# Kernel optimization log

Measured on AMD Instinct MI355X. Metric: run time of the kernel, lower is better.

The kernel has to match this reference:

```python
import jax, jax.numpy as jnp
import numpy as np

NUM_GROUPS = 2
NUM_VARS = 320
CODE_DIM = 256  # per-group dim = 128
TAU = 2.0


def setup_inputs() -> dict:
    key = jax.random.key(0)
    k1, k2, k3, k4 = jax.random.split(key, 4)
    B, S, H = 4, 512, 512
    x = jax.random.normal(k1, (B, S, H), jnp.float32)
    W = jax.random.normal(k2, (H, NUM_GROUPS * NUM_VARS), jnp.float32) * 0.02
    b = jnp.zeros((NUM_GROUPS * NUM_VARS,), jnp.float32)
    codevectors = jax.random.normal(k3, (1, NUM_GROUPS * NUM_VARS, CODE_DIM // NUM_GROUPS), jnp.float32)
    # Gumbel(0,1) noise, matching -log(Exponential(1).sample) in the original
    u = jax.random.uniform(k4, (B * S * NUM_GROUPS, NUM_VARS), jnp.float32, 1e-6, 1.0 - 1e-6)
    gumbels = -jnp.log(-jnp.log(u))
    return {"x": x, "W": W, "b": b, "codevectors": codevectors, "gumbels": gumbels}


def reference(x, W, b, codevectors, gumbels):
    B, S, H = x.shape
    BS = B * S
    logits = x @ W + b                                    # [B, S, G*V]
    l = logits.reshape(BS * NUM_GROUPS, NUM_VARS)         # [BS*G, V]
    # gumbel-softmax, hard=True (straight-through)
    y_soft = jax.nn.softmax((l + gumbels) / TAU, axis=-1)
    idx = jnp.argmax(y_soft, axis=-1)
    y_hard = jax.nn.one_hot(idx, NUM_VARS, dtype=l.dtype)
    codevector_probs = y_hard - jax.lax.stop_gradient(y_soft) + y_soft
    # perplexity over the soft distribution of the raw logits (no gumbel, no tau)
    soft_dist = jax.nn.softmax(l.reshape(BS, NUM_GROUPS, NUM_VARS), axis=-1)
    marg = jnp.mean(soft_dist, axis=0)                    # [G, V]
    perp = jnp.sum(jnp.exp(-jnp.sum(marg * jnp.log(marg + 1e-7), axis=-1)))
    # dense broadcast-multiply-reduce codebook selection (as in the original)
    cp = codevector_probs.reshape(BS, NUM_GROUPS * NUM_VARS)        # [BS, G*V]
    cv = cp[:, :, None] * codevectors                                # [BS, G*V, D/G]
    cv = cv.reshape(BS, NUM_GROUPS, NUM_VARS, -1).sum(axis=-2)      # [BS, G, D/G]
    return cv.reshape(B, S, -1), perp
```

## Files before the change

kernel.cpp:

```cpp
#include <hip/hip_runtime.h>

#define NV 320
#define GV 640
#define DHALF 128
#define BSROWS 2048
#define K_DIM 512
#define LDA 40
#define NRED 40
#define NMT 128

typedef _Float16 half8 __attribute__((ext_vector_type(8)));
typedef float floatx4 __attribute__((ext_vector_type(4)));

#define MFMA16(a, b, c) __builtin_amdgcn_mfma_f32_16x16x32_f16(a, b, c, 0, 0, 0)

__global__ __launch_bounds__(256) void gemm_row_kernel(
    const float* __restrict__ X, const float* __restrict__ W,
    const float* __restrict__ bias, const float* __restrict__ gum,
    const float* __restrict__ cvs, float* __restrict__ out,
    float* __restrict__ part, int* __restrict__ counter) {
  __shared__ _Float16 Ah[2][16 * LDA], Al[2][16 * LDA];
  __shared__ float sm_m[4][16], sm_av[4][16], sm_s[4][16];
  __shared__ int sm_ai[4][16], sm_idx[16];

  const int tid = threadIdx.x;
  const int bid = blockIdx.x;
  if (bid == 0 && tid == 0) *counter = 0;
  const int g = bid & 1;
  const int mtile = bid >> 1;
  const int bm = mtile * 16;
  const int w = tid >> 6, lane = tid & 63;
  const int wcol0 = w * 80;
  const int gn0 = g * NV;

  const int srow = tid >> 4, skc = (tid & 15) << 1;
  const float* Xg = X + (bm + srow) * K_DIM + skc;
  const int sA = srow * LDA + skc;

  const int frow = lane & 15;
  const int rq0 = (lane >> 4) << 2;
  const int fkg = (lane >> 4) << 3;
  const float* Wf = W + gn0 + wcol0 + frow;

  float gv[5][4];
#pragma unroll
  for (int q = 0; q < 4; ++q) {
    const int r = bm + rq0 + q;
    const float* gr = gum + (2 * r + g) * NV + wcol0 + frow;
#pragma unroll
    for (int j = 0; j < 5; ++j) gv[j][q] = gr[j * 16];
  }

  floatx4 acc[5] = {};

  auto stageA = [&](int buf, float2 xv) {
#pragma unroll
    for (int j = 0; j < 2; ++j) {
      float s = ((j == 0) ? xv.x : xv.y) * 64.0f;
      _Float16 h = (_Float16)s;
      Ah[buf][sA + j] = h;
      Al[buf][sA + j] = (_Float16)(s - (float)h);
    }
  };
  auto loadW = [&](int k0, float (&wv)[5][8]) {
#pragma unroll
    for (int j = 0; j < 5; ++j)
#pragma unroll
      for (int kk = 0; kk < 8; ++kk)
        wv[j][kk] = Wf[(k0 + fkg + kk) * GV + j * 16];
  };
  auto computeTile = [&](int buf, const float (&wv)[5][8]) {
    half8 ah = *(const half8*)&Ah[buf][frow * LDA + fkg];
    half8 al = *(const half8*)&Al[buf][frow * LDA + fkg];
#pragma unroll
    for (int j = 0; j < 5; ++j) {
      half8 bh, bl;
#pragma unroll
      for (int kk = 0; kk < 8; ++kk) {
        float s = wv[j][kk] * 1024.0f;
        _Float16 h = (_Float16)s;
        bh[kk] = h;
        bl[kk] = (_Float16)(s - (float)h);
      }
      acc[j] = MFMA16(ah, bh, acc[j]);
      acc[j] = MFMA16(ah, bl, acc[j]);
      acc[j] = MFMA16(al, bh, acc[j]);
    }
  };

  float wvA[5][8], wvB[5][8];
  stageA(0, *(const float2*)(Xg));
  loadW(0, wvA);
  __syncthreads();

  for (int k0 = 0; k0 < K_DIM; k0 += 64) {
    const bool more = (k0 + 64) < K_DIM;

    float2 xv1 = *(const float2*)(Xg + k0 + 32);
    loadW(k0 + 32, wvB);
    computeTile(0, wvA);
    stageA(1, xv1);
    __syncthreads();

    float2 xv2;
    if (more) {
      xv2 = *(const float2*)(Xg + k0 + 64);
      loadW(k0 + 64, wvA);
    }
    computeTile(1, wvB);
    if (more) stageA(0, xv2);
    __syncthreads();
  }

  const float inv = 1.0f / 65536.0f;
#pragma unroll
  for (int j = 0; j < 5; ++j) {
    const float bb = bias[gn0 + wcol0 + j * 16 + frow];
#pragma unroll
    for (int q = 0; q < 4; ++q) acc[j][q] = acc[j][q] * inv + bb;
  }

  float m[4], bv[4];
  int bi[4];
#pragma unroll
  for (int q = 0; q < 4; ++q) {
    float mm = acc[0][q];
    float av = acc[0][q] + gv[0][q];
    int ai = wcol0 + frow;
#pragma unroll
    for (int j = 1; j < 5; ++j) {
      mm = fmaxf(mm, acc[j][q]);
      float a2 = acc[j][q] + gv[j][q];
      if (a2 > av) { av = a2; ai = wcol0 + j * 16 + frow; }
    }
#pragma unroll
    for (int o = 1; o < 16; o <<= 1) {
      mm = fmaxf(mm, __shfl_xor(mm, o));
      float ov = __shfl_xor(av, o);
      int oi = __shfl_xor(ai, o);
      if (ov > av || (ov == av && oi < ai)) { av = ov; ai = oi; }
    }
    m[q] = mm; bv[q] = av; bi[q] = ai;
  }
  if (frow == 0) {
#pragma unroll
    for (int q = 0; q < 4; ++q) {
      sm_m[w][rq0 + q] = m[q];
      sm_av[w][rq0 + q] = bv[q];
      sm_ai[w][rq0 + q] = bi[q];
    }
  }
  __syncthreads();

  float gm[4];
#pragma unroll
  for (int q = 0; q < 4; ++q) {
    const int row = rq0 + q;
    float mm = sm_m[0][row];
    float av = sm_av[0][row];
    int ai = sm_ai[0][row];
#pragma unroll
    for (int ww = 1; ww < 4; ++ww) {
      mm = fmaxf(mm, sm_m[ww][row]);
      float v2 = sm_av[ww][row];
      int i2 = sm_ai[ww][row];
      if (v2 > av || (v2 == av && i2 < ai)) { av = v2; ai = i2; }
    }
    gm[q] = mm;
    if (w == 0 && frow == 0) sm_idx[row] = ai;
  }

  float rs[4];
#pragma unroll
  for (int q = 0; q < 4; ++q) {
    float s = 0.f;
#pragma unroll
    for (int j = 0; j < 5; ++j) {
      float e = expf(acc[j][q] - gm[q]);
      acc[j][q] = e;
      s += e;
    }
#pragma unroll
    for (int o = 1; o < 16; o <<= 1) s += __shfl_xor(s, o);
    rs[q] = s;
  }
  if (frow == 0)
#pragma unroll
    for (int q = 0; q < 4; ++q) sm_s[w][rq0 + q] = rs[q];
  __syncthreads();

  float rinv[4];
#pragma unroll
  for (int q = 0; q < 4; ++q) {
    const int row = rq0 + q;
    rinv[q] = 1.f / ((sm_s[0][row] + sm_s[1][row]) + (sm_s[2][row] + sm_s[3][row]));
  }

#pragma unroll
  for (int j = 0; j < 5; ++j) {
    float p = 0.f;
#pragma unroll
    for (int q = 0; q < 4; ++q) p += acc[j][q] * rinv[q];
    p += __shfl_xor(p, 16);
    p += __shfl_xor(p, 32);
    if (lane < 16) part[(g * NMT + mtile) * NV + wcol0 + j * 16 + lane] = p;
  }

#pragma unroll
  for (int it = 0; it < 2; ++it) {
    const int f4 = tid + it * 256;
    const int row = f4 >> 5;
    const int d = (f4 & 31) << 2;
    const int id = sm_idx[row];
    const float4 v = *(const float4*)(cvs + (g * NV + id) * DHALF + d);
    *(float4*)(out + (bm + row) * 256 + g * DHALF + d) = v;
  }
}

__global__ __launch_bounds__(256) void reduce_perp_kernel(
    const float* __restrict__ part, float* __restrict__ hpart,
    int* __restrict__ counter, float* __restrict__ perpOut) {
  const int t = threadIdx.x;
  const int rg = t >> 4, co = t & 15;
  const int col = blockIdx.x * 16 + co;
  const int g = (col >= NV) ? 1 : 0;
  const int c = col - g * NV;
  float s = 0.f;
  for (int b = rg; b < NMT; b += 16) s += part[(g * NMT + b) * NV + c];
  __shared__ float red[16][16];
  red[rg][co] = s;
  __syncthreads();
  if (t < 16) {
    float cs = 0.f;
#pragma unroll
    for (int j = 0; j < 16; ++j) cs += red[j][t];
    const float mm = cs * (1.0f / BSROWS);
    float h = mm * logf(mm + 1e-7f);
#pragma unroll
    for (int o = 8; o > 0; o >>= 1) h += __shfl_xor(h, o, 16);
    if (t == 0) {
      hpart[blockIdx.x] = h;
      __threadfence();
      const int old = atomicAdd(counter, 1);
      if (old == NRED - 1) {
        __threadfence();
        float h0 = 0.f, h1 = 0.f;
#pragma unroll
        for (int i = 0; i < 20; ++i) h0 += hpart[i];
#pragma unroll
        for (int i = 20; i < 40; ++i) h1 += hpart[i];
        perpOut[0] = expf(-h0) + expf(-h1);
      }
    }
  }
}

extern "C" void kernel_launch(void* const* d_in, const int* in_sizes, int n_in,
                              void* d_out, int out_size, void* d_ws, size_t ws_size,
                              hipStream_t stream) {
  const float* x = (const float*)d_in[0];
  const float* W = (const float*)d_in[1];
  const float* b = (const float*)d_in[2];
  const float* cvs = (const float*)d_in[3];
  const float* gum = (const float*)d_in[4];
  float* out = (float*)d_out;

  float* part = (float*)d_ws;
  float* hpart = part + 2 * NMT * NV;
  int* counter = (int*)(hpart + 64);

  gemm_row_kernel<<<256, 256, 0, stream>>>(x, W, b, gum, cvs, out, part, counter);
  reduce_perp_kernel<<<NRED, 256, 0, stream>>>(part, hpart, counter, out + BSROWS * 256);
}
```

Baseline: 31.44 us.

## Fuse perplexity reduction into GEMM kernel via last-block completion counter

Removes the separate reduction kernel and performs the perplexity reduction in the last block of the main kernel to finish, detected with an atomic counter taken modulo the block count. This eliminates a kernel launch and the gap between kernels. In exchange, the reduction over all partials now runs serially in a single block, and every block pays a fence plus an atomic. The counter is no longer reset and relies on wraparound modulo the block count.

```diff
diff --git a/kernel.cpp b/kernel.cpp
--- a/kernel.cpp
+++ b/kernel.cpp
@@ -6,8 +6,8 @@
 #define BSROWS 2048
 #define K_DIM 512
 #define LDA 40
-#define NRED 40
 #define NMT 128
+#define NBLK 256
 
 typedef _Float16 half8 __attribute__((ext_vector_type(8)));
 typedef float floatx4 __attribute__((ext_vector_type(4)));
@@ -18,14 +18,15 @@
     const float* __restrict__ X, const float* __restrict__ W,
     const float* __restrict__ bias, const float* __restrict__ gum,
     const float* __restrict__ cvs, float* __restrict__ out,
-    float* __restrict__ part, int* __restrict__ counter) {
+    float* __restrict__ part, int* __restrict__ counter,
+    float* __restrict__ perpOut) {
   __shared__ _Float16 Ah[2][16 * LDA], Al[2][16 * LDA];
   __shared__ float sm_m[4][16], sm_av[4][16], sm_s[4][16];
   __shared__ int sm_ai[4][16], sm_idx[16];
+  __shared__ int lastFlag;
 
   const int tid = threadIdx.x;
   const int bid = blockIdx.x;
-  if (bid == 0 && tid == 0) *counter = 0;
   const int g = bid & 1;
   const int mtile = bid >> 1;
   const int bm = mtile * 16;
@@ -215,43 +216,40 @@
     const float4 v = *(const float4*)(cvs + (g * NV + id) * DHALF + d);
     *(float4*)(out + (bm + row) * 256 + g * DHALF + d) = v;
   }
-}
-
-__global__ __launch_bounds__(256) void reduce_perp_kernel(
-    const float* __restrict__ part, float* __restrict__ hpart,
-    int* __restrict__ counter, float* __restrict__ perpOut) {
-  const int t = threadIdx.x;
-  const int rg = t >> 4, co = t & 15;
-  const int col = blockIdx.x * 16 + co;
-  const int g = (col >= NV) ? 1 : 0;
-  const int c = col - g * NV;
-  float s = 0.f;
-  for (int b = rg; b < NMT; b += 16) s += part[(g * NMT + b) * NV + c];
-  __shared__ float red[16][16];
-  red[rg][co] = s;
-  __syncthreads();
-  if (t < 16) {
-    float cs = 0.f;
-#pragma unroll
-    for (int j = 0; j < 16; ++j) cs += red[j][t];
-    const float mm = cs * (1.0f / BSROWS);
-    float h = mm * logf(mm + 1e-7f);
-#pragma unroll
-    for (int o = 8; o > 0; o >>= 1) h += __shfl_xor(h, o, 16);
-    if (t == 0) {
-      hpart[blockIdx.x] = h;
-      __threadfence();
-      const int old = atomicAdd(counter, 1);
-      if (old == NRED - 1) {
-        __threadfence();
-        float h0 = 0.f, h1 = 0.f;
-#pragma unroll
-        for (int i = 0; i < 20; ++i) h0 += hpart[i];
-#pragma unroll
-        for (int i = 20; i < 40; ++i) h1 += hpart[i];
-        perpOut[0] = expf(-h0) + expf(-h1);
+
+  __threadfence();
+  __syncthreads();
+  if (tid == 0) {
+    const int old = atomicAdd(counter, 1);
+    lastFlag = ((old & (NBLK - 1)) == (NBLK - 1)) ? 1 : 0;
+  }
+  __syncthreads();
+
+  if (lastFlag) {
+    __threadfence();
+    float h0 = 0.f, h1 = 0.f;
+#pragma unroll
+    for (int c0 = 0; c0 < GV; c0 += 256) {
+      const int col = c0 + tid;
+      if (col < GV) {
+        const int gg = (col >= NV) ? 1 : 0;
+        const int c = col - gg * NV;
+        float s = 0.f;
+        for (int b = 0; b < NMT; ++b) s += part[(gg * NMT + b) * NV + c];
+        const float mm = s * (1.0f / BSROWS);
+        const float t = mm * logf(mm + 1e-7f);
+        if (gg == 0) h0 += t; else h1 += t;
       }
     }
+    __shared__ float r0[256], r1[256];
+    r0[tid] = h0;
+    r1[tid] = h1;
+    __syncthreads();
+    for (int s = 128; s > 0; s >>= 1) {
+      if (tid < s) { r0[tid] += r0[tid + s]; r1[tid] += r1[tid + s]; }
+      __syncthreads();
+    }
+    if (tid == 0) perpOut[0] = expf(-r0[0]) + expf(-r1[0]);
   }
 }
 
@@ -266,9 +264,8 @@
   float* out = (float*)d_out;
 
   float* part = (float*)d_ws;
-  float* hpart = part + 2 * NMT * NV;
-  int* counter = (int*)(hpart + 64);
-
-  gemm_row_kernel<<<256, 256, 0, stream>>>(x, W, b, gum, cvs, out, part, counter);
-  reduce_perp_kernel<<<NRED, 256, 0, stream>>>(part, hpart, counter, out + BSROWS * 256);
+  int* counter = (int*)(part + 2 * NMT * NV);
+
+  gemm_row_kernel<<<NBLK, 256, 0, stream>>>(x, W, b, gum, cvs, out, part, counter,
+                                            out + BSROWS * 256);
 }
```

Measured after the change: 60.39 us. 1.92x slower.

## Halve rows per block to 8 to double grid size for more parallelism

Applied to the files above, without the earlier changes.

Shrinks each GEMM block's M tile from 16 to 8 rows and doubles the grid from 256 to 512 blocks, so more CUs stay busy on the 256-CU-class GPU. The 16-row MFMA tile is filled by duplicating the 8 rows, which wastes half the MFMA work and repeats every W load per block. The duplicated rows are masked out of the perplexity partial sums. The reduce kernel now has twice as many partials to sum.

```diff
diff --git a/kernel.cpp b/kernel.cpp
--- a/kernel.cpp
+++ b/kernel.cpp
@@ -7,7 +7,7 @@
 #define K_DIM 512
 #define LDA 40
 #define NRED 40
-#define NMT 128
+#define NMT 256
 
 typedef _Float16 half8 __attribute__((ext_vector_type(8)));
 typedef float floatx4 __attribute__((ext_vector_type(4)));
@@ -19,7 +19,7 @@
     const float* __restrict__ bias, const float* __restrict__ gum,
     const float* __restrict__ cvs, float* __restrict__ out,
     float* __restrict__ part, int* __restrict__ counter) {
-  __shared__ _Float16 Ah[2][16 * LDA], Al[2][16 * LDA];
+  __shared__ _Float16 Ah[2][8 * LDA], Al[2][8 * LDA];
   __shared__ float sm_m[4][16], sm_av[4][16], sm_s[4][16];
   __shared__ int sm_ai[4][16], sm_idx[16];
 
@@ -28,24 +28,27 @@
   if (bid == 0 && tid == 0) *counter = 0;
   const int g = bid & 1;
   const int mtile = bid >> 1;
-  const int bm = mtile * 16;
+  const int bm = mtile * 8;
   const int w = tid >> 6, lane = tid & 63;
   const int wcol0 = w * 80;
   const int gn0 = g * NV;
 
-  const int srow = tid >> 4, skc = (tid & 15) << 1;
+  const int srow = tid >> 5, skc = tid & 31;
   const float* Xg = X + (bm + srow) * K_DIM + skc;
   const int sA = srow * LDA + skc;
 
   const int frow = lane & 15;
+  const int arow = frow & 7;
   const int rq0 = (lane >> 4) << 2;
+  const int rq = rq0 & 7;
+  const bool dup = rq0 >= 8;
   const int fkg = (lane >> 4) << 3;
   const float* Wf = W + gn0 + wcol0 + frow;
 
   float gv[5][4];
 #pragma unroll
   for (int q = 0; q < 4; ++q) {
-    const int r = bm + rq0 + q;
+    const int r = bm + rq + q;
     const float* gr = gum + (2 * r + g) * NV + wcol0 + frow;
 #pragma unroll
     for (int j = 0; j < 5; ++j) gv[j][q] = gr[j * 16];
@@ -53,14 +56,11 @@
 
   floatx4 acc[5] = {};
 
-  auto stageA = [&](int buf, float2 xv) {
-#pragma unroll
-    for (int j = 0; j < 2; ++j) {
-      float s = ((j == 0) ? xv.x : xv.y) * 64.0f;
-      _Float16 h = (_Float16)s;
-      Ah[buf][sA + j] = h;
-      Al[buf][sA + j] = (_Float16)(s - (float)h);
-    }
+  auto stageA = [&](int buf, float xv) {
+    float s = xv * 64.0f;
+    _Float16 h = (_Float16)s;
+    Ah[buf][sA] = h;
+    Al[buf][sA] = (_Float16)(s - (float)h);
   };
   auto loadW = [&](int k0, float (&wv)[5][8]) {
 #pragma unroll
@@ -70,8 +70,8 @@
         wv[j][kk] = Wf[(k0 + fkg + kk) * GV + j * 16];
   };
   auto computeTile = [&](int buf, const float (&wv)[5][8]) {
-    half8 ah = *(const half8*)&Ah[buf][frow * LDA + fkg];
-    half8 al = *(const half8*)&Al[buf][frow * LDA + fkg];
+    half8 ah = *(const half8*)&Ah[buf][arow * LDA + fkg];
+    half8 al = *(const half8*)&Al[buf][arow * LDA + fkg];
 #pragma unroll
     for (int j = 0; j < 5; ++j) {
       half8 bh, bl;
@@ -89,22 +89,22 @@
   };
 
   float wvA[5][8], wvB[5][8];
-  stageA(0, *(const float2*)(Xg));
+  stageA(0, *Xg);
   loadW(0, wvA);
   __syncthreads();
 
   for (int k0 = 0; k0 < K_DIM; k0 += 64) {
     const bool more = (k0 + 64) < K_DIM;
 
-    float2 xv1 = *(const float2*)(Xg + k0 + 32);
+    float xv1 = Xg[k0 + 32];
     loadW(k0 + 32, wvB);
     computeTile(0, wvA);
     stageA(1, xv1);
     __syncthreads();
 
-    float2 xv2;
+    float xv2 = 0.f;
     if (more) {
-      xv2 = *(const float2*)(Xg + k0 + 64);
+      xv2 = Xg[k0 + 64];
       loadW(k0 + 64, wvA);
     }
     computeTile(1, wvB);
@@ -200,17 +200,15 @@
   for (int j = 0; j < 5; ++j) {
     float p = 0.f;
 #pragma unroll
-    for (int q = 0; q < 4; ++q) p += acc[j][q] * rinv[q];
+    for (int q = 0; q < 4; ++q) p += dup ? 0.f : acc[j][q] * rinv[q];
     p += __shfl_xor(p, 16);
     p += __shfl_xor(p, 32);
     if (lane < 16) part[(g * NMT + mtile) * NV + wcol0 + j * 16 + lane] = p;
   }
 
-#pragma unroll
-  for (int it = 0; it < 2; ++it) {
-    const int f4 = tid + it * 256;
-    const int row = f4 >> 5;
-    const int d = (f4 & 31) << 2;
+  {
+    const int row = tid >> 5;
+    const int d = (tid & 31) << 2;
     const int id = sm_idx[row];
     const float4 v = *(const float4*)(cvs + (g * NV + id) * DHALF + d);
     *(float4*)(out + (bm + row) * 256 + g * DHALF + d) = v;
@@ -269,6 +267,6 @@
   float* hpart = part + 2 * NMT * NV;
   int* counter = (int*)(hpart + 64);
 
-  gemm_row_kernel<<<256, 256, 0, stream>>>(x, W, b, gum, cvs, out, part, counter);
+  gemm_row_kernel<<<2 * NMT, 256, 0, stream>>>(x, W, b, gum, cvs, out, part, counter);
   reduce_perp_kernel<<<NRED, 256, 0, stream>>>(part, hpart, counter, out + BSROWS * 256);
 }
```

New measurement: 41.49 us. 32.0% more time.
